# Kernel tuning notes

Measured on AMD Instinct MI355X. Metric: run time of the kernel, lower is better.

## Reference

```python
import jax, jax.numpy as jnp
import numpy as np

B, N, C = 4, 2048, 768
H, HD = 12, 64
RANK, ALPHA = 8, 16.0
SCALING = ALPHA / RANK
SCALE = HD ** -0.5


def setup_inputs() -> dict:
    key = jax.random.key(0)
    ks = jax.random.split(key, 10)
    return {
        "x": jax.random.normal(ks[0], (B, N, C), jnp.float32),
        "qkv_weight": jax.random.normal(ks[1], (3 * C, C), jnp.float32) * 0.02,
        "q_bias": jax.random.normal(ks[2], (C,), jnp.float32) * 0.02,
        "v_bias": jax.random.normal(ks[3], (C,), jnp.float32) * 0.02,
        "lora_A_qkv": jax.random.normal(ks[4], (RANK, C), jnp.float32) * 0.02,
        "lora_B_qkv": jax.random.normal(ks[5], (3 * C, RANK), jnp.float32) * 0.02,
        "proj_weight": jax.random.normal(ks[6], (C, C), jnp.float32) * 0.02,
        "proj_bias": jax.random.normal(ks[7], (C,), jnp.float32) * 0.02,
        "lora_A_proj": jax.random.normal(ks[8], (RANK, C), jnp.float32) * 0.02,
        "lora_B_proj": jax.random.normal(ks[9], (C, RANK), jnp.float32) * 0.02,
    }


def reference(x, qkv_weight, q_bias, v_bias, lora_A_qkv, lora_B_qkv,
              proj_weight, proj_bias, lora_A_proj, lora_B_proj):
    # qkv bias = [q_bias, zeros, v_bias]
    qkv_bias = jnp.concatenate([q_bias, jnp.zeros_like(v_bias), v_bias])
    qkv = jnp.einsum('bnc,oc->bno', x, qkv_weight) + qkv_bias  # [B,N,3C]
    # LoRA on qkv: (x @ A^T @ B^T) * scaling
    qkv = qkv + jnp.einsum('bnr,or->bno', jnp.einsum('bnc,rc->bnr', x, lora_A_qkv), lora_B_qkv) * SCALING
    qkv = qkv.reshape(B, N, 3, H, HD).transpose(2, 0, 3, 1, 4)  # [3,B,H,N,HD]
    q, k, v = qkv[0], qkv[1], qkv[2]
    attn = jnp.einsum('bhnd,bhmd->bhnm', q * SCALE, k)  # [B,H,N,N]
    attn = jax.nn.softmax(attn, axis=-1)
    out = jnp.einsum('bhnm,bhmd->bhnd', attn, v)
    out = out.transpose(0, 2, 1, 3).reshape(B, N, C)
    out = jnp.einsum('bnc,oc->bno', out, proj_weight) + proj_bias
    # NOTE: module applies proj LoRA to the OUTPUT of proj (faithful quirk)
    out = out + jnp.einsum('bnr,or->bno', jnp.einsum('bnc,rc->bnr', out, lora_A_proj), lora_B_proj) * SCALING
    return out
```

## Files before the change

kernel.cpp:

```cpp
#include <hip/hip_runtime.h>
#include <cstdint>
#include <cstddef>

typedef __bf16 bf16;
typedef __bf16 bf16x4_t __attribute__((ext_vector_type(4)));
typedef __bf16 bf16x8_t __attribute__((ext_vector_type(8)));
typedef float f32x4_t __attribute__((ext_vector_type(4)));
typedef unsigned int u32;
typedef u32 u32x2_t __attribute__((ext_vector_type(2)));

#define DEV __device__ __forceinline__

static constexpr int CD  = 768;
static constexpr int C3  = 2304;
static constexpr int SEQ = 2048;
static constexpr int NB  = 4;
static constexpr int NH  = 12;
static constexpr int HDM = 64;
static constexpr int BHN = NB * NH;
static constexpr float QSCALE = 0.125f * 1.44269504088896340736f;
static constexpr float DEFER_THR = 4.0f;

DEV void async16(const void* g, void* l) {
  __builtin_amdgcn_global_load_lds(
      (const __attribute__((address_space(1))) void*)g,
      (__attribute__((address_space(3))) void*)l, 16, 0, 0);
}

DEV int swz(int r) { return (r ^ (r >> 2)) & 3; }

DEV u32 pack_bf16(float lo, float hi) {
  unsigned short l = __builtin_bit_cast(unsigned short, (bf16)lo);
  unsigned short h = __builtin_bit_cast(unsigned short, (bf16)hi);
  return ((u32)h << 16) | (u32)l;
}

DEV float max3f(float a, float b, float c) { return fmaxf(fmaxf(a, b), c); }

__global__ void k_cast(const float* __restrict__ x, bf16* __restrict__ o, int n4) {
  int i = blockIdx.x * blockDim.x + threadIdx.x;
  int stride = gridDim.x * blockDim.x;
  for (; i < n4; i += stride) {
    float4 v = reinterpret_cast<const float4*>(x)[i];
    bf16x4_t b;
    b[0] = (bf16)v.x; b[1] = (bf16)v.y; b[2] = (bf16)v.z; b[3] = (bf16)v.w;
    reinterpret_cast<bf16x4_t*>(o)[i] = b;
  }
}

__global__ void k_prep_qkvw(const float* __restrict__ W, const float* __restrict__ Aq,
                            const float* __restrict__ Bq, bf16* __restrict__ We) {
  int idx = blockIdx.x * 256 + threadIdx.x;
  int o = idx / CD, c = idx % CD;
  float s = 0.f;
#pragma unroll
  for (int r = 0; r < 8; ++r) s += Bq[o * 8 + r] * Aq[r * CD + c];
  We[idx] = (bf16)(W[idx] + 2.0f * s);
}

__global__ void k_prep_T(const float* __restrict__ Ap, const float* __restrict__ Wp,
                         float* __restrict__ T) {
  __shared__ float part[4][64];
  const int r = blockIdx.x / 12, cp0 = (blockIdx.x % 12) * 64;
  const int kl = threadIdx.x >> 6, cpl = threadIdx.x & 63;
  float s = 0.f;
  const int c0 = kl * 192;
  for (int c = c0; c < c0 + 192; ++c)
    s += Ap[r * CD + c] * Wp[(size_t)c * CD + cp0 + cpl];
  part[kl][cpl] = s;
  __syncthreads();
  if (threadIdx.x < 64)
    T[r * CD + cp0 + threadIdx.x] = (part[0][threadIdx.x] + part[1][threadIdx.x]) +
                                    (part[2][threadIdx.x] + part[3][threadIdx.x]);
}

__global__ void k_prep_projw(const float* __restrict__ Wp, const float* __restrict__ Bp,
                             const float* __restrict__ T, bf16* __restrict__ We) {
  int idx = blockIdx.x * 256 + threadIdx.x;
  int o = idx / CD, cp = idx % CD;
  float s = 0.f;
#pragma unroll
  for (int r = 0; r < 8; ++r) s += Bp[o * 8 + r] * T[r * CD + cp];
  We[idx] = (bf16)(Wp[idx] + 2.0f * s);
}

__global__ void k_prep_beff(const float* __restrict__ bp, const float* __restrict__ Ap,
                            const float* __restrict__ Bp, float* __restrict__ be) {
  __shared__ float tl[8];
  const int tid = threadIdx.x;
  const int r = tid >> 5, cl = tid & 31;
  float part = 0.f;
  for (int c = cl; c < CD; c += 32) part += Ap[r * CD + c] * bp[c];
#pragma unroll
  for (int d = 1; d < 32; d <<= 1) part += __shfl_xor(part, d);
  if (cl == 0) tl[r] = part;
  __syncthreads();
  for (int o = tid; o < CD; o += 256) {
    float s = 0.f;
#pragma unroll
    for (int rr = 0; rr < 8; ++rr) s += Bp[o * 8 + rr] * tl[rr];
    be[o] = bp[o] + 2.0f * s;
  }
}

template <int MODE>
__global__ __launch_bounds__(256) void k_gemm(
    const bf16* __restrict__ Ag, const bf16* __restrict__ Bg,
    const float* __restrict__ qb, const float* __restrict__ vb,
    bf16* __restrict__ Qo, bf16* __restrict__ Ko, bf16* __restrict__ Vo,
    const float* __restrict__ beff, float* __restrict__ Fo) {
  __shared__ bf16 lds[2][2][128 * 32];
  const int tid = threadIdx.x;
  const int w = tid >> 6, lane = tid & 63;
  const int lr = lane & 15, lg = lane >> 4;
  const int m0 = blockIdx.y * 128, n0 = blockIdx.x * 128;
  const int wm = w >> 1, wn = w & 1;

  const int r0 = tid >> 2, gp0 = tid & 3;
  const int r1 = 64 + r0;
  const bf16* gA0 = Ag + (size_t)(m0 + r0) * CD + (gp0 ^ swz(r0)) * 8;
  const bf16* gA1 = Ag + (size_t)(m0 + r1) * CD + (gp0 ^ swz(r1)) * 8;
  const bf16* gB0 = Bg + (size_t)(n0 + r0) * CD + (gp0 ^ swz(r0)) * 8;
  const bf16* gB1 = Bg + (size_t)(n0 + r1) * CD + (gp0 ^ swz(r1)) * 8;
  const int dd0 = w * 1024, dd1 = 4096 + w * 1024;

  f32x4_t acc[4][4] = {};

  auto stage = [&](int buf, int kof) {
    char* ba = (char*)&lds[buf][0][0];
    char* bb = (char*)&lds[buf][1][0];
    async16(gA0 + kof, ba + dd0);
    async16(gA1 + kof, ba + dd1);
    async16(gB0 + kof, bb + dd0);
    async16(gB1 + kof, bb + dd1);
  };

  stage(0, 0);
  int cur = 0;
  const int NK = CD / 32;
  for (int kt = 0; kt < NK; ++kt) {
    __syncthreads();
    if (kt + 1 < NK) stage(cur ^ 1, (kt + 1) * 32);
    const char* ba = (const char*)&lds[cur][0][0];
    const char* bb = (const char*)&lds[cur][1][0];
    bf16x8_t af[4], bfr[4];
#pragma unroll
    for (int mi = 0; mi < 4; ++mi) {
      int rr = wm * 64 + mi * 16 + lr;
      af[mi] = *(const bf16x8_t*)(ba + rr * 64 + ((lg ^ swz(rr)) * 16));
    }
#pragma unroll
    for (int ni = 0; ni < 4; ++ni) {
      int rr = wn * 64 + ni * 16 + lr;
      bfr[ni] = *(const bf16x8_t*)(bb + rr * 64 + ((lg ^ swz(rr)) * 16));
    }
#pragma unroll
    for (int mi = 0; mi < 4; ++mi)
#pragma unroll
      for (int ni = 0; ni < 4; ++ni)
        acc[mi][ni] = __builtin_amdgcn_mfma_f32_16x16x32_bf16(bfr[ni], af[mi], acc[mi][ni], 0, 0, 0);
    cur ^= 1;
  }

  if (MODE == 0) {
    const int t = n0 / CD;
#pragma unroll
    for (int mi = 0; mi < 4; ++mi) {
      const int m = m0 + wm * 64 + mi * 16 + lr;
      const int b = m >> 11, nn = m & 2047;
#pragma unroll
      for (int ni = 0; ni < 4; ++ni) {
        const int nb = n0 + wn * 64 + ni * 16 + lg * 4;
        const int rem = nb - t * CD;
        const int h = rem >> 6, hd = rem & 63;
        const size_t oa = ((size_t)((b * NH + h) * SEQ + nn)) * HDM + hd;
        bf16x4_t o4;
        if (t == 0) {
          const float4 bias = *(const float4*)(qb + rem);
          o4[0] = (bf16)((acc[mi][ni][0] + bias.x) * QSCALE);
          o4[1] = (bf16)((acc[mi][ni][1] + bias.y) * QSCALE);
          o4[2] = (bf16)((acc[mi][ni][2] + bias.z) * QSCALE);
          o4[3] = (bf16)((acc[mi][ni][3] + bias.w) * QSCALE);
          *(bf16x4_t*)(Qo + oa) = o4;
        } else if (t == 1) {
#pragma unroll
          for (int j = 0; j < 4; ++j) o4[j] = (bf16)acc[mi][ni][j];
          *(bf16x4_t*)(Ko + oa) = o4;
        } else {
          const float4 bias = *(const float4*)(vb + rem);
          o4[0] = (bf16)(acc[mi][ni][0] + bias.x);
          o4[1] = (bf16)(acc[mi][ni][1] + bias.y);
          o4[2] = (bf16)(acc[mi][ni][2] + bias.z);
          o4[3] = (bf16)(acc[mi][ni][3] + bias.w);
          *(bf16x4_t*)(Vo + oa) = o4;
        }
      }
    }
  } else {
#pragma unroll
    for (int mi = 0; mi < 4; ++mi) {
      const int m = m0 + wm * 64 + mi * 16 + lr;
#pragma unroll
      for (int ni = 0; ni < 4; ++ni) {
        const int nb = n0 + wn * 64 + ni * 16 + lg * 4;
        const float4 be4 = *(const float4*)(beff + nb);
        float4 o;
        o.x = acc[mi][ni][0] + be4.x;
        o.y = acc[mi][ni][1] + be4.y;
        o.z = acc[mi][ni][2] + be4.z;
        o.w = acc[mi][ni][3] + be4.w;
        *(float4*)(Fo + (size_t)m * CD + nb) = o;
      }
    }
  }
}

__global__ void k_trv(const bf16* __restrict__ V, bf16* __restrict__ Vt) {
  __shared__ bf16 t[64][72];
  const int bh = blockIdx.y, s0 = blockIdx.x * 64;
  const int tid = threadIdx.x;
  const int row = tid >> 2, cc = (tid & 3) * 16;
  const bf16* src = V + ((size_t)bh * SEQ + s0 + row) * HDM + cc;
  bf16x8_t a = *(const bf16x8_t*)src;
  bf16x8_t b2 = *(const bf16x8_t*)(src + 8);
#pragma unroll
  for (int i = 0; i < 8; ++i) { t[row][cc + i] = a[i]; t[row][cc + 8 + i] = b2[i]; }
  __syncthreads();
  bf16x8_t o0, o1;
#pragma unroll
  for (int i = 0; i < 8; ++i) { o0[i] = t[cc + i][row]; o1[i] = t[cc + 8 + i][row]; }
  bf16* dst = Vt + ((size_t)bh * HDM + row) * SEQ + s0 + cc;
  *(bf16x8_t*)dst = o0;
  *(bf16x8_t*)(dst + 8) = o1;
}

__global__ __launch_bounds__(256, 3) void k_attn(const bf16* __restrict__ Q,
                                                 const bf16* __restrict__ Kg,
                                                 const bf16* __restrict__ Vt,
                                                 bf16* __restrict__ Ao) {
  __shared__ bf16 Kl[2][64 * 64];
  __shared__ bf16 Vl[2][64 * 64];
  __shared__ bf16 P[4][32 * 72];
  const int tid = threadIdx.x;
  const int w = tid >> 6, lane = tid & 63;
  const int lq = lane & 15, lg = lane >> 4;
  const int L = blockIdx.x;
  const int qb = (L >> 3) & 15;
  const int bh = (L & 7) * 6 + (L >> 7);
  const int b = bh / NH, h = bh % NH;
  const int qrow0 = qb * 128 + w * 32;

  const bf16* Qp = Q + ((size_t)bh * SEQ + qrow0) * HDM;
  const bf16* Kp = Kg + (size_t)bh * SEQ * HDM;
  const bf16* Vp = Vt + (size_t)bh * HDM * SEQ;

  const int sr = tid >> 3, scs = tid & 7;
  const int sr2 = sr + 32;
  bf16* kb0 = &Kl[0][w * 512]; bf16* kb1 = &Kl[1][w * 512];
  bf16* vb0 = &Vl[0][w * 512]; bf16* vb1 = &Vl[1][w * 512];

  auto stageKV = [&](int buf, int kb) {
    bf16* kd = buf ? kb1 : kb0;
    bf16* vd = buf ? vb1 : vb0;
    async16(Kp + (size_t)(kb + sr) * HDM + ((scs ^ (sr & 7)) * 8), kd);
    async16(Kp + (size_t)(kb + sr2) * HDM + ((scs ^ (sr2 & 7)) * 8), kd + 2048);
    async16(Vp + (size_t)sr * SEQ + kb + ((scs ^ (sr & 7)) * 8), vd);
    async16(Vp + (size_t)sr2 * SEQ + kb + ((scs ^ (sr2 & 7)) * 8), vd + 2048);
  };

  bf16x8_t qf[2][2];
#pragma unroll
  for (int qh = 0; qh < 2; ++qh)
#pragma unroll
    for (int s = 0; s < 2; ++s)
      qf[qh][s] = *(const bf16x8_t*)(Qp + (size_t)(lq + 16 * qh) * HDM + s * 32 + lg * 8);

  bf16x8_t ones;
#pragma unroll
  for (int j = 0; j < 8; ++j) ones[j] = (bf16)1.0f;

  f32x4_t oacc[2][2][4] = {};
  float mrun[2][2] = {{-1e30f, -1e30f}, {-1e30f, -1e30f}};
  float lsum[2][2] = {{0.f, 0.f}, {0.f, 0.f}};
  bf16* Pl = &P[w][0];
  const int sw = lq & 7;

  stageKV(0, 0);
  int cur = 0;
  for (int kb = 0; kb < SEQ; kb += 64) {
    __syncthreads();
    if (kb + 64 < SEQ) stageKV(cur ^ 1, kb + 64);
    const bf16* Kc = &Kl[cur][0];
    const bf16* Vc = &Vl[cur][0];

    f32x4_t st[2][2][2];
#pragma unroll
    for (int c = 0; c < 2; ++c)
#pragma unroll
      for (int nt = 0; nt < 2; ++nt) {
        const int row = c * 32 + nt * 16 + lq;
        bf16x8_t k0 = *(const bf16x8_t*)(Kc + row * 64 + ((lg ^ sw) * 8));
        bf16x8_t k1 = *(const bf16x8_t*)(Kc + row * 64 + (((4 + lg) ^ sw) * 8));
#pragma unroll
        for (int qh = 0; qh < 2; ++qh) {
          f32x4_t z = {0.f, 0.f, 0.f, 0.f};
          z = __builtin_amdgcn_mfma_f32_16x16x32_bf16(k0, qf[qh][0], z, 0, 0, 0);
          st[c][nt][qh] = __builtin_amdgcn_mfma_f32_16x16x32_bf16(k1, qf[qh][1], z, 0, 0, 0);
        }
      }

#pragma unroll
    for (int c = 0; c < 2; ++c)
#pragma unroll
      for (int qh = 0; qh < 2; ++qh) {
        float m = max3f(st[c][0][qh][0], st[c][0][qh][1], st[c][0][qh][2]);
        float m2 = max3f(st[c][0][qh][3], st[c][1][qh][0], st[c][1][qh][1]);
        m = max3f(m, m2, st[c][1][qh][2]);
        m = fmaxf(m, st[c][1][qh][3]);
        m = fmaxf(m, __shfl_xor(m, 16));
        m = fmaxf(m, __shfl_xor(m, 32));
        if (__any(m > mrun[c][qh] + DEFER_THR)) {
          const float mnew = fmaxf(mrun[c][qh], m);
          const float corr = __builtin_amdgcn_exp2f(mrun[c][qh] - mnew);
          mrun[c][qh] = mnew;
          lsum[c][qh] *= corr;
#pragma unroll
          for (int dt = 0; dt < 4; ++dt)
#pragma unroll
            for (int j = 0; j < 4; ++j) oacc[c][qh][dt][j] *= corr;
        }
#pragma unroll
        for (int nt = 0; nt < 2; ++nt)
#pragma unroll
          for (int j = 0; j < 4; ++j)
            st[c][nt][qh][j] = __builtin_amdgcn_exp2f(st[c][nt][qh][j] - mrun[c][qh]);

#pragma unroll
        for (int nt = 0; nt < 2; ++nt) {
          u32x2_t pw = {pack_bf16(st[c][nt][qh][0], st[c][nt][qh][1]),
                        pack_bf16(st[c][nt][qh][2], st[c][nt][qh][3])};
          *(u32x2_t*)(Pl + (lq + 16 * qh) * 72 + c * 32 + nt * 16 + lg * 4) = pw;
        }
      }

#pragma unroll
    for (int c = 0; c < 2; ++c) {
      bf16x8_t pf[2];
#pragma unroll
      for (int qh = 0; qh < 2; ++qh) {
        pf[qh] = *(const bf16x8_t*)(Pl + (lq + 16 * qh) * 72 + c * 32 + lg * 8);
        const f32x4_t zz = {0.f, 0.f, 0.f, 0.f};
        f32x4_t srow = __builtin_amdgcn_mfma_f32_16x16x32_bf16(ones, pf[qh], zz, 0, 0, 0);
        lsum[c][qh] += srow[0];
      }
#pragma unroll
      for (int dt = 0; dt < 4; ++dt) {
        const int vrow = dt * 16 + lq;
        bf16x8_t vf = *(const bf16x8_t*)(Vc + vrow * 64 + (((c * 4 + lg) ^ sw) * 8));
#pragma unroll
        for (int qh = 0; qh < 2; ++qh)
          oacc[c][qh][dt] = __builtin_amdgcn_mfma_f32_16x16x32_bf16(vf, pf[qh], oacc[c][qh][dt], 0, 0, 0);
      }
    }
    cur ^= 1;
  }

#pragma unroll
  for (int qh = 0; qh < 2; ++qh) {
    const float mm = fmaxf(mrun[0][qh], mrun[1][qh]);
    const float c0 = __builtin_amdgcn_exp2f(mrun[0][qh] - mm);
    const float c1 = __builtin_amdgcn_exp2f(mrun[1][qh] - mm);
    const float inv = 1.0f / (lsum[0][qh] * c0 + lsum[1][qh] * c1);
    bf16* dst = Ao + ((size_t)b * SEQ + qrow0 + lq + 16 * qh) * CD + h * HDM;
#pragma unroll
    for (int dt = 0; dt < 4; ++dt) {
      bf16x4_t o4;
#pragma unroll
      for (int j = 0; j < 4; ++j)
        o4[j] = (bf16)((oacc[0][qh][dt][j] * c0 + oacc[1][qh][dt][j] * c1) * inv);
      *(bf16x4_t*)(dst + dt * 16 + lg * 4) = o4;
    }
  }
}

extern "C" void kernel_launch(void* const* d_in, const int* in_sizes, int n_in,
                              void* d_out, int out_size, void* d_ws, size_t ws_size,
                              hipStream_t stream) {
  const float* x    = (const float*)d_in[0];
  const float* qkvw = (const float*)d_in[1];
  const float* qb   = (const float*)d_in[2];
  const float* vb   = (const float*)d_in[3];
  const float* Aq   = (const float*)d_in[4];
  const float* Bq   = (const float*)d_in[5];
  const float* Wp   = (const float*)d_in[6];
  const float* bp   = (const float*)d_in[7];
  const float* Ap   = (const float*)d_in[8];
  const float* Bp   = (const float*)d_in[9];
  float* out = (float*)d_out;

  char* ws = (char*)d_ws;
  size_t off = 0;
  auto alloc = [&](size_t bytes) {
    void* p = ws + off;
    off += (bytes + 511) & ~size_t(511);
    return p;
  };
  const size_t M = (size_t)NB * SEQ;
  bf16* xb   = (bf16*)alloc(M * CD * 2);
  bf16* Wqe  = (bf16*)alloc((size_t)C3 * CD * 2);
  bf16* Wpe  = (bf16*)alloc((size_t)CD * CD * 2);
  float* T   = (float*)alloc(8 * CD * 4);
  float* be  = (float*)alloc(CD * 4);
  bf16* Qb   = (bf16*)alloc((size_t)BHN * SEQ * HDM * 2);
  bf16* Kb   = (bf16*)alloc((size_t)BHN * SEQ * HDM * 2);
  bf16* Vb   = (bf16*)alloc((size_t)BHN * SEQ * HDM * 2);
  bf16* Vtb  = (bf16*)alloc((size_t)BHN * SEQ * HDM * 2);
  bf16* attn = xb;

  k_cast<<<2048, 256, 0, stream>>>(x, xb, (int)(M * CD / 4));
  k_prep_qkvw<<<(C3 * CD) / 256, 256, 0, stream>>>(qkvw, Aq, Bq, Wqe);
  k_prep_T<<<96, 256, 0, stream>>>(Ap, Wp, T);
  k_prep_projw<<<(CD * CD) / 256, 256, 0, stream>>>(Wp, Bp, T, Wpe);
  k_prep_beff<<<1, 256, 0, stream>>>(bp, Ap, Bp, be);

  k_gemm<0><<<dim3(C3 / 128, M / 128), 256, 0, stream>>>(
      xb, Wqe, qb, vb, Qb, Kb, Vb, nullptr, nullptr);
  k_trv<<<dim3(SEQ / 64, BHN), 256, 0, stream>>>(Vb, Vtb);
  k_attn<<<(SEQ / 128) * BHN, 256, 0, stream>>>(Qb, Kb, Vtb, attn);
  k_gemm<1><<<dim3(CD / 128, M / 128), 256, 0, stream>>>(
      attn, Wpe, nullptr, nullptr, nullptr, nullptr, nullptr, be, out);
}
```

Before: 202.2 us.

## Enlarge QKV GEMM tile to 256x128 and load V fragments directly from global

The QKV projection GEMM becomes a dedicated 512-thread kernel with a 256x128 tile. Each B tile is now shared by twice as many rows, which cuts grid size and B-operand reloads. Separately, the attention kernel no longer stages V through LDS; each wave reads its V fragments straight from global memory every key block. This frees LDS and drops the async V copies, but the V loads become uncoalesced, latency-exposed global reads inside the inner loop.

```diff
diff --git a/kernel.cpp b/kernel.cpp
--- a/kernel.cpp
+++ b/kernel.cpp
@@ -103,11 +103,95 @@
   }
 }
 
-template <int MODE>
-__global__ __launch_bounds__(256) void k_gemm(
+__global__ __launch_bounds__(512) void k_gemm0(
     const bf16* __restrict__ Ag, const bf16* __restrict__ Bg,
     const float* __restrict__ qb, const float* __restrict__ vb,
-    bf16* __restrict__ Qo, bf16* __restrict__ Ko, bf16* __restrict__ Vo,
+    bf16* __restrict__ Qo, bf16* __restrict__ Ko, bf16* __restrict__ Vo) {
+  __shared__ bf16 lds[2][(256 + 128) * 32];
+  const int tid = threadIdx.x;
+  const int w = tid >> 6, lane = tid & 63;
+  const int lr = lane & 15, lg = lane >> 4;
+  const int m0 = blockIdx.y * 256, n0 = blockIdx.x * 128;
+  const int wm = w >> 1, wn = w & 1;
+
+  const int r0 = tid >> 2, gp0 = tid & 3;
+  const bf16* gA0 = Ag + (size_t)(m0 + r0) * CD + (gp0 ^ swz(r0)) * 8;
+  const bf16* gA1 = Ag + (size_t)(m0 + 128 + r0) * CD + (gp0 ^ swz(r0)) * 8;
+  const bf16* gB0 = Bg + (size_t)(n0 + r0) * CD + (gp0 ^ swz(r0)) * 8;
+
+  f32x4_t acc[4][4] = {};
+
+  auto stage = [&](int buf, int kof) {
+    char* base = (char*)&lds[buf][0];
+    async16(gA0 + kof, base + w * 1024);
+    async16(gA1 + kof, base + 8192 + w * 1024);
+    async16(gB0 + kof, base + 16384 + w * 1024);
+  };
+
+  stage(0, 0);
+  int cur = 0;
+  const int NK = CD / 32;
+  for (int kt = 0; kt < NK; ++kt) {
+    __syncthreads();
+    if (kt + 1 < NK) stage(cur ^ 1, (kt + 1) * 32);
+    const char* ba = (const char*)&lds[cur][0];
+    const char* bb = ba + 16384;
+    bf16x8_t af[4], bfr[4];
+#pragma unroll
+    for (int mi = 0; mi < 4; ++mi) {
+      int rr = wm * 64 + mi * 16 + lr;
+      af[mi] = *(const bf16x8_t*)(ba + rr * 64 + ((lg ^ swz(rr)) * 16));
+    }
+#pragma unroll
+    for (int ni = 0; ni < 4; ++ni) {
+      int rr = wn * 64 + ni * 16 + lr;
+      bfr[ni] = *(const bf16x8_t*)(bb + rr * 64 + ((lg ^ swz(rr)) * 16));
+    }
+#pragma unroll
+    for (int mi = 0; mi < 4; ++mi)
+#pragma unroll
+      for (int ni = 0; ni < 4; ++ni)
+        acc[mi][ni] = __builtin_amdgcn_mfma_f32_16x16x32_bf16(bfr[ni], af[mi], acc[mi][ni], 0, 0, 0);
+    cur ^= 1;
+  }
+
+  const int t = n0 / CD;
+#pragma unroll
+  for (int mi = 0; mi < 4; ++mi) {
+    const int m = m0 + wm * 64 + mi * 16 + lr;
+    const int b = m >> 11, nn = m & 2047;
+#pragma unroll
+    for (int ni = 0; ni < 4; ++ni) {
+      const int nb = n0 + wn * 64 + ni * 16 + lg * 4;
+      const int rem = nb - t * CD;
+      const int h = rem >> 6, hd = rem & 63;
+      const size_t oa = ((size_t)((b * NH + h) * SEQ + nn)) * HDM + hd;
+      bf16x4_t o4;
+      if (t == 0) {
+        const float4 bias = *(const float4*)(qb + rem);
+        o4[0] = (bf16)((acc[mi][ni][0] + bias.x) * QSCALE);
+        o4[1] = (bf16)((acc[mi][ni][1] + bias.y) * QSCALE);
+        o4[2] = (bf16)((acc[mi][ni][2] + bias.z) * QSCALE);
+        o4[3] = (bf16)((acc[mi][ni][3] + bias.w) * QSCALE);
+        *(bf16x4_t*)(Qo + oa) = o4;
+      } else if (t == 1) {
+#pragma unroll
+        for (int j = 0; j < 4; ++j) o4[j] = (bf16)acc[mi][ni][j];
+        *(bf16x4_t*)(Ko + oa) = o4;
+      } else {
+        const float4 bias = *(const float4*)(vb + rem);
+        o4[0] = (bf16)(acc[mi][ni][0] + bias.x);
+        o4[1] = (bf16)(acc[mi][ni][1] + bias.y);
+        o4[2] = (bf16)(acc[mi][ni][2] + bias.z);
+        o4[3] = (bf16)(acc[mi][ni][3] + bias.w);
+        *(bf16x4_t*)(Vo + oa) = o4;
+      }
+    }
+  }
+}
+
+__global__ __launch_bounds__(256) void k_gemm1(
+    const bf16* __restrict__ Ag, const bf16* __restrict__ Bg,
     const float* __restrict__ beff, float* __restrict__ Fo) {
   __shared__ bf16 lds[2][2][128 * 32];
   const int tid = threadIdx.x;
@@ -162,55 +246,19 @@
     cur ^= 1;
   }
 
-  if (MODE == 0) {
-    const int t = n0 / CD;
-#pragma unroll
-    for (int mi = 0; mi < 4; ++mi) {
-      const int m = m0 + wm * 64 + mi * 16 + lr;
-      const int b = m >> 11, nn = m & 2047;
-#pragma unroll
-      for (int ni = 0; ni < 4; ++ni) {
-        const int nb = n0 + wn * 64 + ni * 16 + lg * 4;
-        const int rem = nb - t * CD;
-        const int h = rem >> 6, hd = rem & 63;
-        const size_t oa = ((size_t)((b * NH + h) * SEQ + nn)) * HDM + hd;
-        bf16x4_t o4;
-        if (t == 0) {
-          const float4 bias = *(const float4*)(qb + rem);
-          o4[0] = (bf16)((acc[mi][ni][0] + bias.x) * QSCALE);
-          o4[1] = (bf16)((acc[mi][ni][1] + bias.y) * QSCALE);
-          o4[2] = (bf16)((acc[mi][ni][2] + bias.z) * QSCALE);
-          o4[3] = (bf16)((acc[mi][ni][3] + bias.w) * QSCALE);
-          *(bf16x4_t*)(Qo + oa) = o4;
-        } else if (t == 1) {
-#pragma unroll
-          for (int j = 0; j < 4; ++j) o4[j] = (bf16)acc[mi][ni][j];
-          *(bf16x4_t*)(Ko + oa) = o4;
-        } else {
-          const float4 bias = *(const float4*)(vb + rem);
-          o4[0] = (bf16)(acc[mi][ni][0] + bias.x);
-          o4[1] = (bf16)(acc[mi][ni][1] + bias.y);
-          o4[2] = (bf16)(acc[mi][ni][2] + bias.z);
-          o4[3] = (bf16)(acc[mi][ni][3] + bias.w);
-          *(bf16x4_t*)(Vo + oa) = o4;
-        }
-      }
-    }
-  } else {
-#pragma unroll
-    for (int mi = 0; mi < 4; ++mi) {
-      const int m = m0 + wm * 64 + mi * 16 + lr;
-#pragma unroll
-      for (int ni = 0; ni < 4; ++ni) {
-        const int nb = n0 + wn * 64 + ni * 16 + lg * 4;
-        const float4 be4 = *(const float4*)(beff + nb);
-        float4 o;
-        o.x = acc[mi][ni][0] + be4.x;
-        o.y = acc[mi][ni][1] + be4.y;
-        o.z = acc[mi][ni][2] + be4.z;
-        o.w = acc[mi][ni][3] + be4.w;
-        *(float4*)(Fo + (size_t)m * CD + nb) = o;
-      }
+#pragma unroll
+  for (int mi = 0; mi < 4; ++mi) {
+    const int m = m0 + wm * 64 + mi * 16 + lr;
+#pragma unroll
+    for (int ni = 0; ni < 4; ++ni) {
+      const int nb = n0 + wn * 64 + ni * 16 + lg * 4;
+      const float4 be4 = *(const float4*)(beff + nb);
+      float4 o;
+      o.x = acc[mi][ni][0] + be4.x;
+      o.y = acc[mi][ni][1] + be4.y;
+      o.z = acc[mi][ni][2] + be4.z;
+      o.w = acc[mi][ni][3] + be4.w;
+      *(float4*)(Fo + (size_t)m * CD + nb) = o;
     }
   }
 }
@@ -239,7 +287,6 @@
                                                  const bf16* __restrict__ Vt,
                                                  bf16* __restrict__ Ao) {
   __shared__ bf16 Kl[2][64 * 64];
-  __shared__ bf16 Vl[2][64 * 64];
   __shared__ bf16 P[4][32 * 72];
   const int tid = threadIdx.x;
   const int w = tid >> 6, lane = tid & 63;
@@ -257,15 +304,11 @@
   const int sr = tid >> 3, scs = tid & 7;
   const int sr2 = sr + 32;
   bf16* kb0 = &Kl[0][w * 512]; bf16* kb1 = &Kl[1][w * 512];
-  bf16* vb0 = &Vl[0][w * 512]; bf16* vb1 = &Vl[1][w * 512];
-
-  auto stageKV = [&](int buf, int kb) {
+
+  auto stageK = [&](int buf, int kb) {
     bf16* kd = buf ? kb1 : kb0;
-    bf16* vd = buf ? vb1 : vb0;
     async16(Kp + (size_t)(kb + sr) * HDM + ((scs ^ (sr & 7)) * 8), kd);
     async16(Kp + (size_t)(kb + sr2) * HDM + ((scs ^ (sr2 & 7)) * 8), kd + 2048);
-    async16(Vp + (size_t)sr * SEQ + kb + ((scs ^ (sr & 7)) * 8), vd);
-    async16(Vp + (size_t)sr2 * SEQ + kb + ((scs ^ (sr2 & 7)) * 8), vd + 2048);
   };
 
   bf16x8_t qf[2][2];
@@ -285,13 +328,19 @@
   bf16* Pl = &P[w][0];
   const int sw = lq & 7;
 
-  stageKV(0, 0);
+  stageK(0, 0);
   int cur = 0;
   for (int kb = 0; kb < SEQ; kb += 64) {
     __syncthreads();
-    if (kb + 64 < SEQ) stageKV(cur ^ 1, kb + 64);
+    if (kb + 64 < SEQ) stageK(cur ^ 1, kb + 64);
     const bf16* Kc = &Kl[cur][0];
-    const bf16* Vc = &Vl[cur][0];
+
+    bf16x8_t vf[2][4];
+#pragma unroll
+    for (int c = 0; c < 2; ++c)
+#pragma unroll
+      for (int dt = 0; dt < 4; ++dt)
+        vf[c][dt] = *(const bf16x8_t*)(Vp + (size_t)(dt * 16 + lq) * SEQ + kb + c * 32 + lg * 8);
 
     f32x4_t st[2][2][2];
 #pragma unroll
@@ -354,13 +403,10 @@
         lsum[c][qh] += srow[0];
       }
 #pragma unroll
-      for (int dt = 0; dt < 4; ++dt) {
-        const int vrow = dt * 16 + lq;
-        bf16x8_t vf = *(const bf16x8_t*)(Vc + vrow * 64 + (((c * 4 + lg) ^ sw) * 8));
+      for (int dt = 0; dt < 4; ++dt)
 #pragma unroll
         for (int qh = 0; qh < 2; ++qh)
-          oacc[c][qh][dt] = __builtin_amdgcn_mfma_f32_16x16x32_bf16(vf, pf[qh], oacc[c][qh][dt], 0, 0, 0);
-      }
+          oacc[c][qh][dt] = __builtin_amdgcn_mfma_f32_16x16x32_bf16(vf[c][dt], pf[qh], oacc[c][qh][dt], 0, 0, 0);
     }
     cur ^= 1;
   }
@@ -423,10 +469,9 @@
   k_prep_projw<<<(CD * CD) / 256, 256, 0, stream>>>(Wp, Bp, T, Wpe);
   k_prep_beff<<<1, 256, 0, stream>>>(bp, Ap, Bp, be);
 
-  k_gemm<0><<<dim3(C3 / 128, M / 128), 256, 0, stream>>>(
-      xb, Wqe, qb, vb, Qb, Kb, Vb, nullptr, nullptr);
+  k_gemm0<<<dim3(C3 / 128, M / 256), 512, 0, stream>>>(
+      xb, Wqe, qb, vb, Qb, Kb, Vb);
   k_trv<<<dim3(SEQ / 64, BHN), 256, 0, stream>>>(Vb, Vtb);
   k_attn<<<(SEQ / 128) * BHN, 256, 0, stream>>>(Qb, Kb, Vtb, attn);
-  k_gemm<1><<<dim3(CD / 128, M / 128), 256, 0, stream>>>(
-      attn, Wpe, nullptr, nullptr, nullptr, nullptr, nullptr, be, out);
-}
+  k_gemm1<<<dim3(CD / 128, M / 128), 256, 0, stream>>>(attn, Wpe, be, out);
+}
```

Result: slower. 243.5 us (+20.4%).
